# Performance work log

Hardware: AMD Instinct MI355X
Metric: run time of the kernel (lower is better)

Reference implementation:

```python
import jax, jax.numpy as jnp
import numpy as np

BT, N = 4, 2048
FIN, FOUT = 512, 128          # GGE in/out; FOUT == PPI output (GAGA constraint)
PIN, POUT = 256, 128          # PPIGE in/out
HEAD = 4
K = POUT // HEAD              # per-head dim = 32
NEG_SLOPE = 0.2
MASK_VAL = -1e30


def setup_inputs() -> dict:
    key = jax.random.key(0)
    ks = jax.random.split(key, 24)
    s = 0.05
    inp = {}
    inp["a"] = jax.random.normal(ks[0], (BT, FIN), jnp.float32)
    inp["bio_a"] = jax.random.normal(ks[1], (BT, N, PIN), jnp.float32)
    inp["A"] = jax.random.randint(ks[2], (BT, N, N), 0, 2, jnp.int32)
    inp["b"] = jax.random.normal(ks[3], (BT, FIN), jnp.float32)
    inp["bio_b"] = jax.random.normal(ks[4], (BT, N, PIN), jnp.float32)
    inp["B"] = jax.random.randint(ks[5], (BT, N, N), 0, 2, jnp.int32)
    # PPIGE_GAT params (shared across both graph branches)
    inp["initW"] = jax.random.normal(ks[6], (POUT, PIN), jnp.float32) * s
    inp["initb"] = jnp.zeros((POUT,), jnp.float32)
    inp["projW"] = jax.random.normal(ks[7], (POUT, POUT), jnp.float32) * s  # no bias
    inp["attw"] = jax.random.normal(ks[8], (HEAD, 2 * K), jnp.float32) * s  # per-head [2k]->1
    inp["attb"] = jnp.zeros((HEAD,), jnp.float32)
    # GGE params
    inp["ggeW1"] = jax.random.normal(ks[9], (128, FIN), jnp.float32) * s
    inp["ggeb1"] = jnp.zeros((128,), jnp.float32)
    inp["ggeW2"] = jax.random.normal(ks[10], (FOUT, 128), jnp.float32) * s
    inp["ggeb2"] = jnp.zeros((FOUT,), jnp.float32)
    # LED params (hidden = FOUT)
    inp["convW"] = jax.random.normal(ks[11], (2 * FOUT, 2 * FOUT), jnp.float32) * s  # k=1 conv
    inp["convb"] = jnp.zeros((2 * FOUT,), jnp.float32)
    inp["ledW1"] = jax.random.normal(ks[12], (FOUT, 4 * FOUT), jnp.float32) * s
    inp["ledb1"] = jnp.zeros((FOUT,), jnp.float32)
    inp["ledW2"] = jax.random.normal(ks[13], (2, FOUT), jnp.float32) * s
    inp["ledb2"] = jnp.zeros((2,), jnp.float32)
    return inp


def _gat_layer(x, adj_mask, projW, attw, attb):
    # x: [B,N,POUT]; adj_mask: [B,N,N] bool
    Bt, n, _ = x.shape
    xh = (x @ projW.T).reshape(Bt, n, HEAD, K).transpose(0, 2, 1, 3)  # [B,h,N,k]
    # score(i,j) = leaky_relu(w1.x_i + w2.x_j + b)  (equivalent to Linear on concat)
    s1 = jnp.einsum('bhnk,hk->bhn', xh, attw[:, :K])
    s2 = jnp.einsum('bhnk,hk->bhn', xh, attw[:, K:])
    scores = jax.nn.leaky_relu(
        s1[..., :, None] + s2[..., None, :] + attb[None, :, None, None], NEG_SLOPE)
    scores = jnp.where(adj_mask[:, None], scores, MASK_VAL)
    att = jax.nn.softmax(scores, axis=-1)                     # [B,h,N,N]
    out = jax.nn.relu(att @ xh)                               # [B,h,N,k]
    return out.transpose(0, 2, 1, 3).reshape(Bt, n, HEAD * K)


def _ppige(bio, adj, initW, initb, projW, attw, attb):
    x = bio @ initW.T + initb
    return _gat_layer(x, adj > 0, projW, attw, attb) + x      # residual; dropout=eval


def _gge(a, W1, b1, W2, b2):
    h = jax.nn.relu(a @ W1.T + b1)
    return jax.nn.relu(h @ W2.T + b2)


def _gaga(G, h):
    # G: [B,N,D], h: [B,D]
    att = jax.nn.softmax(jnp.einsum('bnd,bd->bn', G, h), axis=-1)
    return jnp.einsum('bnd,bn->bd', G, att)


def _led(ea, eb, convW, convb, W1, b1, W2, b2):
    # pointwise conv over the length-2 stack [ea, eb], then maxpool over length
    cnn = jnp.maximum(ea @ convW.T + convb, eb @ convW.T + convb)  # [B,2D]
    x = jax.nn.relu(jnp.concatenate([cnn, ea - eb], axis=1) @ W1.T + b1)
    return x @ W2.T + b2


def reference(a, bio_a, A, b, bio_b, B,
              initW, initb, projW, attw, attb,
              ggeW1, ggeb1, ggeW2, ggeb2,
              convW, convb, ledW1, ledb1, ledW2, ledb2):
    G_a = _ppige(bio_a, A, initW, initb, projW, attw, attb)
    G_b = _ppige(bio_b, B, initW, initb, projW, attw, attb)
    h_a = _gge(a, ggeW1, ggeb1, ggeW2, ggeb2)
    h_b = _gge(b, ggeW1, ggeb1, ggeW2, ggeb2)
    e_a = jnp.concatenate([h_a, _gaga(G_a, h_a)], axis=-1)
    e_b = jnp.concatenate([h_b, _gaga(G_b, h_b)], axis=-1)
    logits = _led(e_a, e_b, convW, convb, ledW1, ledb1, ledW2, ledb2)
    return jax.nn.log_softmax(logits, axis=-1)
```

## Files before the change

kernel.cpp:

```cpp
#include <hip/hip_runtime.h>
#include <hip/hip_bf16.h>
#include <math.h>

#define NN 2048
#define NEG 0.2f
#define LOG2E 1.44269504f

typedef short bf16x8 __attribute__((ext_vector_type(8)));
typedef float f32x16 __attribute__((ext_vector_type(16)));

__device__ __forceinline__ float dot4(float4 a, float4 b) {
  return a.x * b.x + a.y * b.y + a.z * b.z + a.w * b.w;
}

__device__ __forceinline__ unsigned short bfbits(float f) {
  union { __hip_bfloat16 b; unsigned short u; } c;
  c.b = __float2bfloat16(f);
  return c.u;
}

template <int VM>
__device__ __forceinline__ void waitv() {
  if constexpr (VM == 0) asm volatile("s_waitcnt vmcnt(0)" ::: "memory");
  else if constexpr (VM == 1) asm volatile("s_waitcnt vmcnt(1)" ::: "memory");
  else if constexpr (VM == 2) asm volatile("s_waitcnt vmcnt(2)" ::: "memory");
  else asm volatile("s_waitcnt vmcnt(3)" ::: "memory");
}

__device__ __forceinline__ void stage_frag(const unsigned short* g, char* l) {
  __builtin_amdgcn_global_load_lds(
      (const __attribute__((address_space(1))) unsigned int*)g,
      (__attribute__((address_space(3))) unsigned int*)l, 16, 0, 0);
}

__global__ __launch_bounds__(256) void k1_init(const float* __restrict__ bioA,
                                               const float* __restrict__ bioB,
                                               const float* __restrict__ W,
                                               const float* __restrict__ bias,
                                               float* __restrict__ xout) {
  __shared__ float As[32][36];
  __shared__ float Ws[32][132];
  const int t = threadIdx.x;
  const int m0 = blockIdx.x * 32;
  const float* A = (m0 < 8192) ? bioA : bioB;
  const int arow0 = (m0 < 8192) ? m0 : (m0 - 8192);
  const int og = t & 31, ig = t >> 5;
  float acc[4][4] = {};
  for (int kt = 0; kt < 256; kt += 32) {
    __syncthreads();
    {
      const int r = t >> 3, kq = t & 7;
      const float4 v = *(const float4*)&A[(arow0 + r) * 256 + kt + kq * 4];
      As[kq * 4 + 0][r] = v.x; As[kq * 4 + 1][r] = v.y;
      As[kq * 4 + 2][r] = v.z; As[kq * 4 + 3][r] = v.w;
    }
#pragma unroll
    for (int u = 0; u < 4; ++u) {
      const int f = u * 256 + t;
      const int o = f >> 3, kq = f & 7;
      const float4 v = *(const float4*)&W[o * 256 + kt + kq * 4];
      Ws[kq * 4 + 0][o] = v.x; Ws[kq * 4 + 1][o] = v.y;
      Ws[kq * 4 + 2][o] = v.z; Ws[kq * 4 + 3][o] = v.w;
    }
    __syncthreads();
#pragma unroll
    for (int kk = 0; kk < 32; ++kk) {
      const float4 a4 = *(const float4*)&As[kk][ig * 4];
      const float4 w4 = *(const float4*)&Ws[kk][og * 4];
      const float av[4] = {a4.x, a4.y, a4.z, a4.w};
      const float wv[4] = {w4.x, w4.y, w4.z, w4.w};
#pragma unroll
      for (int ii = 0; ii < 4; ++ii)
#pragma unroll
        for (int jj = 0; jj < 4; ++jj) acc[ii][jj] += av[ii] * wv[jj];
    }
  }
  const float4 b4 = *(const float4*)&bias[og * 4];
#pragma unroll
  for (int ii = 0; ii < 4; ++ii) {
    const int row = m0 + ig * 4 + ii;
    float4 o4;
    o4.x = acc[ii][0] + b4.x; o4.y = acc[ii][1] + b4.y;
    o4.z = acc[ii][2] + b4.z; o4.w = acc[ii][3] + b4.w;
    *(float4*)&xout[row * 128 + og * 4] = o4;
  }
}

__global__ __launch_bounds__(256) void k2_proj(const float* __restrict__ x,
                                               const float* __restrict__ W,
                                               const float* __restrict__ attw,
                                               unsigned short* __restrict__ xhT2,
                                               float* __restrict__ s1,
                                               float* __restrict__ s2) {
  __shared__ float As[32][36];
  __shared__ float Ws[32][132];
  const int t = threadIdx.x;
  const int m0 = blockIdx.x * 32;
  const int og = t & 31, ig = t >> 5;
  float acc[4][4] = {};
  for (int kt = 0; kt < 128; kt += 32) {
    __syncthreads();
    {
      const int r = t >> 3, kq = t & 7;
      const float4 v = *(const float4*)&x[(m0 + r) * 128 + kt + kq * 4];
      As[kq * 4 + 0][r] = v.x; As[kq * 4 + 1][r] = v.y;
      As[kq * 4 + 2][r] = v.z; As[kq * 4 + 3][r] = v.w;
    }
#pragma unroll
    for (int u = 0; u < 4; ++u) {
      const int f = u * 256 + t;
      const int o = f >> 3, kq = f & 7;
      const float4 v = *(const float4*)&W[o * 128 + kt + kq * 4];
      Ws[kq * 4 + 0][o] = v.x; Ws[kq * 4 + 1][o] = v.y;
      Ws[kq * 4 + 2][o] = v.z; Ws[kq * 4 + 3][o] = v.w;
    }
    __syncthreads();
#pragma unroll
    for (int kk = 0; kk < 32; ++kk) {
      const float4 a4 = *(const float4*)&As[kk][ig * 4];
      const float4 w4 = *(const float4*)&Ws[kk][og * 4];
      const float av[4] = {a4.x, a4.y, a4.z, a4.w};
      const float wv[4] = {w4.x, w4.y, w4.z, w4.w};
#pragma unroll
      for (int ii = 0; ii < 4; ++ii)
#pragma unroll
        for (int jj = 0; jj < 4; ++jj) acc[ii][jj] += av[ii] * wv[jj];
    }
  }
  const int h = og >> 3;
  const int k4i = (og & 7) * 4;
  const int g = m0 >> 13;
  const int bb = (m0 >> 11) & 3;
  const int gb = g * 4 + bb;
  const int n0 = (m0 & 2047) + ig * 4;
  const float4 w1 = *(const float4*)&attw[h * 64 + k4i];
  const float4 w2 = *(const float4*)&attw[h * 64 + 32 + k4i];
  float p1[4], p2[4];
#pragma unroll
  for (int ii = 0; ii < 4; ++ii) {
    float4 v;
    v.x = acc[ii][0]; v.y = acc[ii][1]; v.z = acc[ii][2]; v.w = acc[ii][3];
    p1[ii] = dot4(v, w1);
    p2[ii] = dot4(v, w2);
  }
  {
    const int mtile = n0 >> 4, jslot = (n0 >> 3) & 1, j8 = n0 & 7;
    const int base2 = ((((gb * 4 + h) * 128 + mtile) * 2 + jslot) * 32) * 8 + j8;
#pragma unroll
    for (int jj = 0; jj < 4; ++jj) {
      const int kin = k4i + jj;
      ushort4 u;
      u.x = bfbits(acc[0][jj]); u.y = bfbits(acc[1][jj]);
      u.z = bfbits(acc[2][jj]); u.w = bfbits(acc[3][jj]);
      *(ushort4*)&xhT2[base2 + kin * 8] = u;
    }
  }
#pragma unroll
  for (int s = 1; s < 8; s <<= 1) {
#pragma unroll
    for (int ii = 0; ii < 4; ++ii) {
      p1[ii] += __shfl_xor(p1[ii], s);
      p2[ii] += __shfl_xor(p2[ii], s);
    }
  }
  if ((og & 7) == 0) {
#pragma unroll
    for (int ii = 0; ii < 4; ++ii) {
      s1[(gb * 4 + h) * NN + n0 + ii] = p1[ii];
      s2[(gb * 4 + h) * NN + n0 + ii] = p2[ii];
    }
  }
}

__global__ __launch_bounds__(512) void k3_attn(const unsigned short* __restrict__ xhT2,
                                               const float* __restrict__ s1w,
                                               const float* __restrict__ s2w,
                                               const int* __restrict__ adjA,
                                               const int* __restrict__ adjB,
                                               const float* __restrict__ attb,
                                               const float* __restrict__ x,
                                               float* __restrict__ G) {
  __shared__ __align__(16) unsigned char smem3[75008];
  unsigned int* adjL = (unsigned int*)smem3;
  float* s2L = (float*)(smem3 + 8448);
  float* denR = (float*)(smem3 + 41216);
  char* bufs = (char*)(smem3 + 42240);
  float* accR = (float*)smem3;

  const int t = threadIdx.x;
  const int wave = t >> 6, lane = t & 63;
  const int blk = blockIdx.x;
  const int g = blk >> 8, b = (blk >> 6) & 3;
  const int i0 = (blk & 63) * 32;
  const int gb = g * 4 + b;
  const int* adj = (g ? adjB : adjA) + (b * NN + i0) * NN;
  {
    const float* s2g = s2w + gb * 4 * NN;
#pragma unroll
    for (int u = 0; u < 4; ++u) {
      const int idx = u * 2048 + t * 4;
      float4 v = *(const float4*)&s2g[idx];
      v.x *= LOG2E; v.y *= LOG2E; v.z *= LOG2E; v.w *= LOG2E;
      *(float4*)&s2L[idx] = v;
    }
  }
#pragma unroll
  for (int r4 = 0; r4 < 4; ++r4) {
    const int r = wave * 4 + r4;
    const int* arow = adj + r * NN;
#pragma unroll 4
    for (int w = 0; w < 32; ++w) {
      const int av = arow[w * 64 + lane];
      const unsigned long long m = __ballot(av > 0);
      if (lane < 2) adjL[r * 66 + 2 * w + lane] = (unsigned int)(m >> (32 * lane));
    }
  }
  __syncthreads();

  const int h = wave & 3;
  const int jhalf = wave >> 2;
  const int jlo = jhalf * 1024;
  const int i = lane & 31;
  const int jslot = lane >> 5;
  const float sc1v = (s1w[(gb * 4 + h) * NN + i0 + i] + attb[h]) * LOG2E;
  const unsigned short* bbase = xhT2 + (gb * 4 + h) * 65536 + jhalf * 32768 + lane * 8;
  char* wrb = bufs + wave * 4096;
  const char* rdb = wrb + lane * 16;
  f32x16 acc = {0.f, 0.f, 0.f, 0.f, 0.f, 0.f, 0.f, 0.f,
                0.f, 0.f, 0.f, 0.f, 0.f, 0.f, 0.f, 0.f};
  float den = 0.f;
  stage_frag(bbase + 0 * 512, wrb + 0 * 1024);
  stage_frag(bbase + 1 * 512, wrb + 1 * 1024);
  stage_frag(bbase + 2 * 512, wrb + 2 * 1024);

#define K3_STEP(MM, VM, DOSTAGE)                                              \
  {                                                                           \
    if (DOSTAGE)                                                              \
      stage_frag(bbase + ((MM) + 3) * 512, wrb + (((MM) + 3) & 3) * 1024);    \
    waitv<VM>();                                                              \
    const bf16x8 bcur = *(const bf16x8*)(rdb + ((MM) & 3) * 1024);            \
    const int j0 = jlo + 16 * (MM) + jslot * 8;                               \
    const unsigned int wbits = adjL[i * 66 + ((jlo + 16 * (MM)) >> 5)];       \
    const unsigned int bits8 = wbits >> ((((MM) & 1) * 16) + jslot * 8);      \
    const float4 s2a = *(const float4*)&s2L[h * 2048 + j0];                   \
    const float4 s2b = *(const float4*)&s2L[h * 2048 + j0 + 4];               \
    const float sv[8] = {s2a.x, s2a.y, s2a.z, s2a.w,                          \
                         s2b.x, s2b.y, s2b.z, s2b.w};                         \
    union { bf16x8 v; unsigned short u[8]; } af;                              \
    float dsum = 0.f;                                                         \
    _Pragma("unroll")                                                         \
    for (int e = 0; e < 8; ++e) {                                             \
      float s = sc1v + sv[e];                                                 \
      s = fmaxf(s, NEG * s);                                                  \
      float pe = __builtin_amdgcn_exp2f(s);                                   \
      pe = ((bits8 >> e) & 1u) ? pe : 0.f;                                    \
      af.u[e] = bfbits(pe);                                                   \
      dsum += pe;                                                             \
    }                                                                         \
    den += dsum;                                                              \
    acc = __builtin_amdgcn_mfma_f32_32x32x16_bf16(af.v, bcur, acc, 0, 0, 0);  \
  }

#pragma unroll 4
  for (int m = 0; m <= 60; ++m) K3_STEP(m, 3, true);
  K3_STEP(61, 2, false);
  K3_STEP(62, 1, false);
  K3_STEP(63, 0, false);
#undef K3_STEP

  den += __shfl_xor(den, 32);
  if (lane < 32) denR[(h * 2 + jhalf) * 32 + lane] = den;
  __syncthreads();
  if (jhalf == 1) {
#pragma unroll
    for (int r = 0; r < 16; ++r) accR[(h * 16 + r) * 65 + lane] = acc[r];
  }
  __syncthreads();
  if (jhalf == 0) {
#pragma unroll
    for (int r = 0; r < 16; ++r) {
      const int row = (r & 3) + 8 * (r >> 2) + 4 * jslot;
      const float dinv = 1.f / (denR[(h * 2 + 0) * 32 + row] + denR[(h * 2 + 1) * 32 + row]);
      const int off = (gb * NN + i0 + row) * 128 + h * 32 + i;
      const float av = acc[r] + accR[(h * 16 + r) * 65 + lane];
      G[off] = fmaxf(av * dinv, 0.f) + x[off];
    }
  }
}

__global__ __launch_bounds__(256) void k4h_gge(const float* __restrict__ a_in,
                                               const float* __restrict__ b_in,
                                               const float* __restrict__ ggeW1,
                                               const float* __restrict__ ggeb1,
                                               const float* __restrict__ ggeW2,
                                               const float* __restrict__ ggeb2,
                                               float* __restrict__ hvbuf,
                                               float* __restrict__ e) {
  __shared__ float inL[512];
  __shared__ float h1L[128];
  const int t = threadIdx.x;
  const int wave = t >> 6, lane = t & 63;
  const int g = blockIdx.x >> 2, b = blockIdx.x & 3;
  const int gb2 = g * 4 + b;
  const float* inp = (g ? b_in : a_in) + b * 512;
  if (t < 128) *(float4*)&inL[t * 4] = *(const float4*)&inp[t * 4];
  __syncthreads();
  for (int p = 0; p < 16; ++p) {
    const int o0 = p * 8 + wave * 2;
    const float* w0 = &ggeW1[o0 * 512 + lane * 8];
    const float* w1 = &ggeW1[(o0 + 1) * 512 + lane * 8];
    const float4 i0v = *(const float4*)&inL[lane * 8];
    const float4 i1v = *(const float4*)&inL[lane * 8 + 4];
    float s0 = dot4(*(const float4*)&w0[0], i0v) + dot4(*(const float4*)&w0[4], i1v);
    float s1v = dot4(*(const float4*)&w1[0], i0v) + dot4(*(const float4*)&w1[4], i1v);
#pragma unroll
    for (int s = 1; s < 64; s <<= 1) { s0 += __shfl_xor(s0, s); s1v += __shfl_xor(s1v, s); }
    if (lane == 0) {
      h1L[o0] = fmaxf(s0 + ggeb1[o0], 0.f);
      h1L[o0 + 1] = fmaxf(s1v + ggeb1[o0 + 1], 0.f);
    }
  }
  __syncthreads();
  for (int p = 0; p < 16; ++p) {
    const int o0 = p * 8 + wave * 2;
    const float2 w0 = *(const float2*)&ggeW2[o0 * 128 + lane * 2];
    const float2 w1 = *(const float2*)&ggeW2[(o0 + 1) * 128 + lane * 2];
    const float2 hvv = *(const float2*)&h1L[lane * 2];
    float s0 = w0.x * hvv.x + w0.y * hvv.y;
    float s1v = w1.x * hvv.x + w1.y * hvv.y;
#pragma unroll
    for (int s = 1; s < 64; s <<= 1) { s0 += __shfl_xor(s0, s); s1v += __shfl_xor(s1v, s); }
    if (lane == 0) {
      const float v0 = fmaxf(s0 + ggeb2[o0], 0.f);
      const float v1 = fmaxf(s1v + ggeb2[o0 + 1], 0.f);
      hvbuf[gb2 * 128 + o0] = v0;
      hvbuf[gb2 * 128 + o0 + 1] = v1;
      e[gb2 * 256 + o0] = v0;
      e[gb2 * 256 + o0 + 1] = v1;
    }
  }
}

__global__ __launch_bounds__(256) void k4a_logits(const float* __restrict__ G,
                                                  const float* __restrict__ hv,
                                                  float* __restrict__ lg) {
  const int t = threadIdx.x;
  const int wave = t >> 6, lane = t & 63;
  const int gb = blockIdx.x >> 4, chunk = blockIdx.x & 15;
  const float2 hvv = *(const float2*)&hv[gb * 128 + lane * 2];
  const float* Gb = G + gb * NN * 128;
  const int nbase = chunk * 128 + wave * 32;
  for (int q = 0; q < 32; ++q) {
    const int n = nbase + q;
    const float2 gv = *(const float2*)&Gb[n * 128 + lane * 2];
    float part = gv.x * hvv.x + gv.y * hvv.y;
#pragma unroll
    for (int s = 1; s < 64; s <<= 1) part += __shfl_xor(part, s);
    if (lane == 0) lg[gb * NN + n] = part;
  }
}

__global__ __launch_bounds__(256) void k4b_reduce(const float* __restrict__ lg,
                                                  float* __restrict__ mz) {
  __shared__ float red[256];
  const int t = threadIdx.x;
  const int gb = blockIdx.x;
  const float* l = lg + gb * NN;
  float m = -1e30f;
  for (int n = t; n < NN; n += 256) m = fmaxf(m, l[n]);
  red[t] = m; __syncthreads();
#pragma unroll
  for (int s = 128; s > 0; s >>= 1) {
    if (t < s) red[t] = fmaxf(red[t], red[t + s]);
    __syncthreads();
  }
  const float mx = red[0]; __syncthreads();
  float z = 0.f;
  for (int n = t; n < NN; n += 256) z += __expf(l[n] - mx);
  red[t] = z; __syncthreads();
#pragma unroll
  for (int s = 128; s > 0; s >>= 1) {
    if (t < s) red[t] += red[t + s];
    __syncthreads();
  }
  if (t == 0) { mz[gb * 2] = mx; mz[gb * 2 + 1] = red[0]; }
}

__global__ __launch_bounds__(256) void k4c_wsum(const float* __restrict__ G,
                                                const float* __restrict__ lg,
                                                const float* __restrict__ mz,
                                                float* __restrict__ wsum) {
  __shared__ float pL[128];
  __shared__ float red[2][128];
  const int t = threadIdx.x;
  const int gb = blockIdx.x >> 4, chunk = blockIdx.x & 15;
  const float mx = mz[gb * 2];
  if (t < 128) pL[t] = __expf(lg[gb * NN + chunk * 128 + t] - mx);
  __syncthreads();
  const int d = t & 127, half = t >> 7;
  const float* Gb = G + (gb * NN + chunk * 128 + half * 64) * 128;
  float acc = 0.f;
  for (int q = 0; q < 64; ++q) acc += pL[half * 64 + q] * Gb[q * 128 + d];
  red[half][d] = acc;
  __syncthreads();
  if (t < 128) wsum[(gb * 16 + chunk) * 128 + t] = red[0][t] + red[1][t];
}

__global__ __launch_bounds__(128) void k4d_final(const float* __restrict__ wsum,
                                                 const float* __restrict__ mz,
                                                 float* __restrict__ e) {
  const int t = threadIdx.x;
  const int gb = blockIdx.x;
  float s = 0.f;
#pragma unroll
  for (int c = 0; c < 16; ++c) s += wsum[(gb * 16 + c) * 128 + t];
  e[gb * 256 + 128 + t] = s / mz[gb * 2 + 1];
}

__global__ __launch_bounds__(256) void k5_led(const float* __restrict__ e,
                                              const float* __restrict__ convW,
                                              const float* __restrict__ convb,
                                              const float* __restrict__ ledW1,
                                              const float* __restrict__ ledb1,
                                              const float* __restrict__ ledW2,
                                              const float* __restrict__ ledb2,
                                              float* __restrict__ out) {
  __shared__ float eaL[256], ebL[256], uL[512], xL[128], lgL[2];
  const int t = threadIdx.x;
  const int wave = t >> 6, lane = t & 63;
  const int bt = blockIdx.x;
  if (t < 64) {
    *(float4*)&eaL[t * 4] = *(const float4*)&e[bt * 256 + t * 4];
    *(float4*)&ebL[t * 4] = *(const float4*)&e[(4 + bt) * 256 + t * 4];
  }
  __syncthreads();
  uL[256 + t] = eaL[t] - ebL[t];
  const float4 ea4 = *(const float4*)&eaL[lane * 4];
  const float4 eb4 = *(const float4*)&ebL[lane * 4];
  for (int p = 0; p < 32; ++p) {
    const int o0 = p * 8 + wave * 2;
    const float4 w0 = *(const float4*)&convW[o0 * 256 + lane * 4];
    const float4 w1 = *(const float4*)&convW[(o0 + 1) * 256 + lane * 4];
    float sa0 = dot4(w0, ea4), sb0 = dot4(w0, eb4);
    float sa1 = dot4(w1, ea4), sb1 = dot4(w1, eb4);
#pragma unroll
    for (int s = 1; s < 64; s <<= 1) {
      sa0 += __shfl_xor(sa0, s); sb0 += __shfl_xor(sb0, s);
      sa1 += __shfl_xor(sa1, s); sb1 += __shfl_xor(sb1, s);
    }
    if (lane == 0) {
      const float c0 = convb[o0], c1 = convb[o0 + 1];
      uL[o0] = fmaxf(sa0 + c0, sb0 + c0);
      uL[o0 + 1] = fmaxf(sa1 + c1, sb1 + c1);
    }
  }
  __syncthreads();
  for (int p = 0; p < 16; ++p) {
    const int o0 = p * 8 + wave * 2;
    const float* w0 = &ledW1[o0 * 512 + lane * 8];
    const float* w1 = &ledW1[(o0 + 1) * 512 + lane * 8];
    const float4 u0 = *(const float4*)&uL[lane * 8];
    const float4 u1 = *(const float4*)&uL[lane * 8 + 4];
    float s0 = dot4(*(const float4*)&w0[0], u0) + dot4(*(const float4*)&w0[4], u1);
    float s1v = dot4(*(const float4*)&w1[0], u0) + dot4(*(const float4*)&w1[4], u1);
#pragma unroll
    for (int s = 1; s < 64; s <<= 1) { s0 += __shfl_xor(s0, s); s1v += __shfl_xor(s1v, s); }
    if (lane == 0) {
      xL[o0] = fmaxf(s0 + ledb1[o0], 0.f);
      xL[o0 + 1] = fmaxf(s1v + ledb1[o0 + 1], 0.f);
    }
  }
  __syncthreads();
  if (wave < 2) {
    const float2 w = *(const float2*)&ledW2[wave * 128 + lane * 2];
    const float2 xv = *(const float2*)&xL[lane * 2];
    float s0 = w.x * xv.x + w.y * xv.y;
#pragma unroll
    for (int s = 1; s < 64; s <<= 1) s0 += __shfl_xor(s0, s);
    if (lane == 0) lgL[wave] = s0 + ledb2[wave];
  }
  __syncthreads();
  if (t == 0) {
    const float l0 = lgL[0], l1 = lgL[1];
    const float m = fmaxf(l0, l1);
    const float za = __expf(l0 - m) + __expf(l1 - m);
    const float lz = __logf(za);
    out[bt * 2 + 0] = l0 - m - lz;
    out[bt * 2 + 1] = l1 - m - lz;
  }
}

extern "C" void kernel_launch(void* const* d_in, const int* in_sizes, int n_in,
                              void* d_out, int out_size, void* d_ws, size_t ws_size,
                              hipStream_t stream) {
  (void)in_sizes; (void)n_in; (void)out_size; (void)ws_size;
  const float* a     = (const float*)d_in[0];
  const float* bioA  = (const float*)d_in[1];
  const int*   A     = (const int*)d_in[2];
  const float* b     = (const float*)d_in[3];
  const float* bioB  = (const float*)d_in[4];
  const int*   B     = (const int*)d_in[5];
  const float* initW = (const float*)d_in[6];
  const float* initb = (const float*)d_in[7];
  const float* projW = (const float*)d_in[8];
  const float* attw  = (const float*)d_in[9];
  const float* attb  = (const float*)d_in[10];
  const float* ggeW1 = (const float*)d_in[11];
  const float* ggeb1 = (const float*)d_in[12];
  const float* ggeW2 = (const float*)d_in[13];
  const float* ggeb2 = (const float*)d_in[14];
  const float* convW = (const float*)d_in[15];
  const float* convb = (const float*)d_in[16];
  const float* ledW1 = (const float*)d_in[17];
  const float* ledb1 = (const float*)d_in[18];
  const float* ledW2 = (const float*)d_in[19];
  const float* ledb2 = (const float*)d_in[20];

  float* ws = (float*)d_ws;
  float*          x    = ws;
  unsigned short* xhT2 = (unsigned short*)(ws + 2097152);
  float*          s1   = ws + 3145728;
  float*          s2   = ws + 3211264;
  float*          G    = ws + 3276800;
  float*          lg   = ws + 5373952;
  float*          wsum = ws + 5390336;
  float*          mz   = ws + 5406720;
  float*          hv   = ws + 5406736;
  float*          e    = ws + 5407760;
  float* out = (float*)d_out;

  k1_init<<<512, 256, 0, stream>>>(bioA, bioB, initW, initb, x);
  k2_proj<<<512, 256, 0, stream>>>(x, projW, attw, xhT2, s1, s2);
  k3_attn<<<512, 512, 0, stream>>>(xhT2, s1, s2, A, B, attb, x, G);
  k4h_gge<<<8, 256, 0, stream>>>(a, b, ggeW1, ggeb1, ggeW2, ggeb2, hv, e);
  k4a_logits<<<128, 256, 0, stream>>>(G, hv, lg);
  k4b_reduce<<<8, 256, 0, stream>>>(lg, mz);
  k4c_wsum<<<128, 256, 0, stream>>>(G, lg, mz, wsum);
  k4d_final<<<8, 128, 0, stream>>>(wsum, mz, e);
  k5_led<<<4, 256, 0, stream>>>(e, convW, convb, ledW1, ledb1, ledW2, ledb2, out);
}
```

Before: 205.8 us.

## Load attention B fragments directly into registers with double-buffered prefetch

Replaces the LDS staging of bf16 value fragments (global_load_lds with manual vmcnt waits) with direct global-to-register loads, double-buffered in groups of four and ordered with sched_barriers. This removes 32KB of LDS, which could allow more blocks per CU, and drops the LDS read per step. The adjacency prologue is also changed to issue all 32 row loads per row before the ballots, raising memory-level parallelism. In exchange it needs more VGPRs for the in-flight fragments and the adjacency array, and direct global loads may expose more latency.

```diff
diff --git a/kernel.cpp b/kernel.cpp
--- a/kernel.cpp
+++ b/kernel.cpp
@@ -17,20 +17,6 @@
   union { __hip_bfloat16 b; unsigned short u; } c;
   c.b = __float2bfloat16(f);
   return c.u;
-}
-
-template <int VM>
-__device__ __forceinline__ void waitv() {
-  if constexpr (VM == 0) asm volatile("s_waitcnt vmcnt(0)" ::: "memory");
-  else if constexpr (VM == 1) asm volatile("s_waitcnt vmcnt(1)" ::: "memory");
-  else if constexpr (VM == 2) asm volatile("s_waitcnt vmcnt(2)" ::: "memory");
-  else asm volatile("s_waitcnt vmcnt(3)" ::: "memory");
-}
-
-__device__ __forceinline__ void stage_frag(const unsigned short* g, char* l) {
-  __builtin_amdgcn_global_load_lds(
-      (const __attribute__((address_space(1))) unsigned int*)g,
-      (__attribute__((address_space(3))) unsigned int*)l, 16, 0, 0);
 }
 
 __global__ __launch_bounds__(256) void k1_init(const float* __restrict__ bioA,
@@ -172,73 +158,32 @@
   }
 }
 
-__global__ __launch_bounds__(512) void k3_attn(const unsigned short* __restrict__ xhT2,
-                                               const float* __restrict__ s1w,
-                                               const float* __restrict__ s2w,
-                                               const int* __restrict__ adjA,
-                                               const int* __restrict__ adjB,
-                                               const float* __restrict__ attb,
-                                               const float* __restrict__ x,
-                                               float* __restrict__ G) {
-  __shared__ __align__(16) unsigned char smem3[75008];
-  unsigned int* adjL = (unsigned int*)smem3;
-  float* s2L = (float*)(smem3 + 8448);
-  float* denR = (float*)(smem3 + 41216);
-  char* bufs = (char*)(smem3 + 42240);
-  float* accR = (float*)smem3;
-
-  const int t = threadIdx.x;
-  const int wave = t >> 6, lane = t & 63;
-  const int blk = blockIdx.x;
-  const int g = blk >> 8, b = (blk >> 6) & 3;
-  const int i0 = (blk & 63) * 32;
-  const int gb = g * 4 + b;
-  const int* adj = (g ? adjB : adjA) + (b * NN + i0) * NN;
-  {
-    const float* s2g = s2w + gb * 4 * NN;
-#pragma unroll
-    for (int u = 0; u < 4; ++u) {
-      const int idx = u * 2048 + t * 4;
-      float4 v = *(const float4*)&s2g[idx];
-      v.x *= LOG2E; v.y *= LOG2E; v.z *= LOG2E; v.w *= LOG2E;
-      *(float4*)&s2L[idx] = v;
-    }
-  }
-#pragma unroll
-  for (int r4 = 0; r4 < 4; ++r4) {
-    const int r = wave * 4 + r4;
-    const int* arow = adj + r * NN;
-#pragma unroll 4
-    for (int w = 0; w < 32; ++w) {
-      const int av = arow[w * 64 + lane];
-      const unsigned long long m = __ballot(av > 0);
-      if (lane < 2) adjL[r * 66 + 2 * w + lane] = (unsigned int)(m >> (32 * lane));
-    }
-  }
-  __syncthreads();
-
-  const int h = wave & 3;
-  const int jhalf = wave >> 2;
-  const int jlo = jhalf * 1024;
-  const int i = lane & 31;
-  const int jslot = lane >> 5;
-  const float sc1v = (s1w[(gb * 4 + h) * NN + i0 + i] + attb[h]) * LOG2E;
-  const unsigned short* bbase = xhT2 + (gb * 4 + h) * 65536 + jhalf * 32768 + lane * 8;
-  char* wrb = bufs + wave * 4096;
-  const char* rdb = wrb + lane * 16;
-  f32x16 acc = {0.f, 0.f, 0.f, 0.f, 0.f, 0.f, 0.f, 0.f,
-                0.f, 0.f, 0.f, 0.f, 0.f, 0.f, 0.f, 0.f};
-  float den = 0.f;
-  stage_frag(bbase + 0 * 512, wrb + 0 * 1024);
-  stage_frag(bbase + 1 * 512, wrb + 1 * 1024);
-  stage_frag(bbase + 2 * 512, wrb + 2 * 1024);
-
-#define K3_STEP(MM, VM, DOSTAGE)                                              \
+#define K3_PROLOGUE                                                           \
   {                                                                           \
-    if (DOSTAGE)                                                              \
-      stage_frag(bbase + ((MM) + 3) * 512, wrb + (((MM) + 3) & 3) * 1024);    \
-    waitv<VM>();                                                              \
-    const bf16x8 bcur = *(const bf16x8*)(rdb + ((MM) & 3) * 1024);            \
+    const float* s2g = s2w + gb * 4 * NN;                                     \
+    _Pragma("unroll")                                                         \
+    for (int u = 0; u < 4; ++u) {                                             \
+      const int idx = u * 2048 + t * 4;                                       \
+      float4 v = *(const float4*)&s2g[idx];                                   \
+      v.x *= LOG2E; v.y *= LOG2E; v.z *= LOG2E; v.w *= LOG2E;                 \
+      *(float4*)&s2L[idx] = v;                                                \
+    }                                                                         \
+  }                                                                           \
+  _Pragma("unroll")                                                           \
+  for (int r4 = 0; r4 < 4; ++r4) {                                            \
+    const int r = wave * 4 + r4;                                              \
+    const int* arow = adj + r * NN;                                           \
+    int av[32];                                                               \
+    _Pragma("unroll")                                                         \
+    for (int w = 0; w < 32; ++w) av[w] = arow[w * 64 + lane];                 \
+    _Pragma("unroll")                                                         \
+    for (int w = 0; w < 32; ++w) {                                            \
+      const unsigned long long mm = __ballot(av[w] > 0);                      \
+      if (lane < 2) adjL[r * 66 + 2 * w + lane] = (unsigned int)(mm >> (32 * lane)); \
+    }                                                                         \
+  }
+
+#define K3_SCORE_BODY(MM)                                                     \
     const int j0 = jlo + 16 * (MM) + jslot * 8;                               \
     const unsigned int wbits = adjL[i * 66 + ((jlo + 16 * (MM)) >> 5)];       \
     const unsigned int bits8 = wbits >> ((((MM) & 1) * 16) + jslot * 8);      \
@@ -257,16 +202,79 @@
       af.u[e] = bfbits(pe);                                                   \
       dsum += pe;                                                             \
     }                                                                         \
-    den += dsum;                                                              \
-    acc = __builtin_amdgcn_mfma_f32_32x32x16_bf16(af.v, bcur, acc, 0, 0, 0);  \
-  }
-
-#pragma unroll 4
-  for (int m = 0; m <= 60; ++m) K3_STEP(m, 3, true);
-  K3_STEP(61, 2, false);
-  K3_STEP(62, 1, false);
-  K3_STEP(63, 0, false);
-#undef K3_STEP
+    den += dsum;
+
+__global__ __launch_bounds__(512) void k3_attn(const unsigned short* __restrict__ xhT2,
+                                               const float* __restrict__ s1w,
+                                               const float* __restrict__ s2w,
+                                               const int* __restrict__ adjA,
+                                               const int* __restrict__ adjB,
+                                               const float* __restrict__ attb,
+                                               const float* __restrict__ x,
+                                               float* __restrict__ G) {
+  __shared__ __align__(16) unsigned char smem3[42240];
+  unsigned int* adjL = (unsigned int*)smem3;
+  float* s2L = (float*)(smem3 + 8448);
+  float* denR = (float*)(smem3 + 41216);
+  float* accR = (float*)smem3;
+
+  const int t = threadIdx.x;
+  const int wave = t >> 6, lane = t & 63;
+  const int blk = blockIdx.x;
+  const int g = blk >> 8, b = (blk >> 6) & 3;
+  const int i0 = (blk & 63) * 32;
+  const int gb = g * 4 + b;
+  const int* adj = (g ? adjB : adjA) + (b * NN + i0) * NN;
+  K3_PROLOGUE
+  __syncthreads();
+
+  const int h = wave & 3;
+  const int jhalf = wave >> 2;
+  const int jlo = jhalf * 1024;
+  const int i = lane & 31;
+  const int jslot = lane >> 5;
+  const float sc1v = (s1w[(gb * 4 + h) * NN + i0 + i] + attb[h]) * LOG2E;
+  const unsigned short* bbase = xhT2 + (gb * 4 + h) * 65536 + jhalf * 32768 + lane * 8;
+  f32x16 acc = {0.f, 0.f, 0.f, 0.f, 0.f, 0.f, 0.f, 0.f,
+                0.f, 0.f, 0.f, 0.f, 0.f, 0.f, 0.f, 0.f};
+  float den = 0.f;
+
+#define K3_CSTEP(RB, MM)                                                      \
+  {                                                                           \
+    K3_SCORE_BODY(MM)                                                         \
+    acc = __builtin_amdgcn_mfma_f32_32x32x16_bf16(af.v, RB, acc, 0, 0, 0);    \
+  }
+
+  bf16x8 ba0 = *(const bf16x8*)&bbase[0 * 512];
+  bf16x8 ba1 = *(const bf16x8*)&bbase[1 * 512];
+  bf16x8 ba2 = *(const bf16x8*)&bbase[2 * 512];
+  bf16x8 ba3 = *(const bf16x8*)&bbase[3 * 512];
+  __builtin_amdgcn_sched_barrier(0);
+  for (int mb = 0; mb < 64; mb += 8) {
+    bf16x8 bb0 = *(const bf16x8*)&bbase[(mb + 4) * 512];
+    bf16x8 bb1 = *(const bf16x8*)&bbase[(mb + 5) * 512];
+    bf16x8 bb2 = *(const bf16x8*)&bbase[(mb + 6) * 512];
+    bf16x8 bb3 = *(const bf16x8*)&bbase[(mb + 7) * 512];
+    __builtin_amdgcn_sched_barrier(0);
+    K3_CSTEP(ba0, mb + 0)
+    K3_CSTEP(ba1, mb + 1)
+    K3_CSTEP(ba2, mb + 2)
+    K3_CSTEP(ba3, mb + 3)
+    __builtin_amdgcn_sched_barrier(0);
+    if (mb < 56) {
+      ba0 = *(const bf16x8*)&bbase[(mb + 8) * 512];
+      ba1 = *(const bf16x8*)&bbase[(mb + 9) * 512];
+      ba2 = *(const bf16x8*)&bbase[(mb + 10) * 512];
+      ba3 = *(const bf16x8*)&bbase[(mb + 11) * 512];
+    }
+    __builtin_amdgcn_sched_barrier(0);
+    K3_CSTEP(bb0, mb + 4)
+    K3_CSTEP(bb1, mb + 5)
+    K3_CSTEP(bb2, mb + 6)
+    K3_CSTEP(bb3, mb + 7)
+    __builtin_amdgcn_sched_barrier(0);
+  }
+#undef K3_CSTEP
 
   den += __shfl_xor(den, 32);
   if (lane < 32) denR[(h * 2 + jhalf) * 32 + lane] = den;
@@ -282,8 +290,8 @@
       const int row = (r & 3) + 8 * (r >> 2) + 4 * jslot;
       const float dinv = 1.f / (denR[(h * 2 + 0) * 32 + row] + denR[(h * 2 + 1) * 32 + row]);
       const int off = (gb * NN + i0 + row) * 128 + h * 32 + i;
-      const float av = acc[r] + accR[(h * 16 + r) * 65 + lane];
-      G[off] = fmaxf(av * dinv, 0.f) + x[off];
+      const float av2 = acc[r] + accR[(h * 16 + r) * 65 + lane];
+      G[off] = fmaxf(av2 * dinv, 0.f) + x[off];
     }
   }
 }
```

Result: faster. 178.2 us (-13.4%).
